# Optimization experiments

Measured on AMD Instinct MI355X. Metric: run time of the kernel, lower is better.

The kernel has to match this reference:

```python
import jax, jax.numpy as jnp
import numpy as np


def _hfft3(x):
    # sequential Hermitian FFT along the 3 spatial axes; each axis n -> 2*(n-1)
    for ax in (2, 3, 4):
        x = jnp.fft.hfft(x, axis=ax)
    return x


def _ihfft3(x):
    # sequential inverse Hermitian FFT; ihfft requires real input, so take real
    # part before each application (mirrors numpy semantics on the original code)
    for ax in (2, 3, 4):
        x = jnp.fft.ihfft(jnp.real(x), axis=ax)
    return x


def setup_inputs() -> dict:
    key = jax.random.key(0)
    k1, k2 = jax.random.split(key)
    B, Cin, Cout = 4, 32, 32
    D1 = D2 = D3 = 64
    m1 = m2 = m3 = 16
    scale = 1.0 / (Cin * Cout)
    x = jax.random.normal(k1, (B, Cin, D1, D2, D3), dtype=jnp.float32)
    weights1 = scale * jax.random.uniform(k2, (Cin, Cout, m1, m2, m3), dtype=jnp.float32)
    return {"x": x, "weights1": weights1}


def reference(x, weights1):
    B = x.shape[0]
    D1, D2, D3 = x.shape[2], x.shape[3], x.shape[4]
    Cout = weights1.shape[1]
    m1, m2, m3 = weights1.shape[2], weights1.shape[3], weights1.shape[4]

    # 3D Hartley-style transform: [B,Cin,2(D1-1),2(D2-1),2(D3-1)] real
    x_ht = _hfft3(x)

    # mode truncation + channel mixing on low modes only
    low = jnp.einsum("bixyz,ioxyz->boxyz", x_ht[:, :, :m1, :m2, :m3], weights1)

    out_ht = jnp.zeros((B, Cout, D1, D2, D3 // 2 + 1), dtype=x.dtype)
    out_ht = out_ht.at[:, :, :m1, :m2, :m3].set(low)

    # inverse transform -> complex [B,Cout,D1//2+1,D2//2+1,(D3//2+1)//2+1]
    out = _ihfft3(out_ht)
    # return real/imag stacked so output is real-valued
    return jnp.stack([out.real, out.imag], axis=-1)
```

## Files before the change

kernel.cpp:

```cpp
#include <hip/hip_runtime.h>
#include <hip/hip_bf16.h>


#define PI2 6.283185307179586476925f

__global__ void k_init(float* __restrict__ Tmat, float* __restrict__ cA,
                       float* __restrict__ cB, float* __restrict__ sB) {
    int t = blockIdx.x * 256 + threadIdx.x;
    if (t < 1024) {
        int k = t >> 6, j = t & 63;
        float w = (j == 0 || j == 63) ? 1.f : 2.f;
        int r = (j * k) % 126;
        Tmat[t] = w * cosf(PI2 * (float)r / 126.f);
    }
    if (t < 528) {
        int p = t >> 4, j = t & 15;
        int r = (j * p) % 64;
        cA[t] = cosf(PI2 * (float)r / 64.f) * (1.f / 64.f);
    }
    if (t < 272) {
        int p = t >> 4, j = t & 15;
        int r = (j * p) % 33;
        float a = PI2 * (float)r / 33.f;
        cB[t] = cosf(a) * (1.f / 33.f);
        sB[t] = sinf(a) * (1.f / 33.f);
    }
}

__global__ __launch_bounds__(256) void k_fwd12(const float* __restrict__ x,
                                               const float* __restrict__ Tmat,
                                               float* __restrict__ A2) {
    __shared__ float xt[64 * 68];
    __shared__ float Ts[16 * 68];
    __shared__ float tmp[16 * 68];
    const int j1 = blockIdx.x, bc = blockIdx.y;
    const int t = threadIdx.x;

    float4* xt4 = (float4*)xt;
    float4* Ts4 = (float4*)Ts;
    const float4* xg = (const float4*)(x + ((size_t)bc * 64 + j1) * 4096);
    for (int c = t; c < 1024; c += 256) {
        int j2 = c >> 4, q = c & 15;
        xt4[j2 * 17 + q] = xg[c];
    }
    if (t < 256) {
        const float4* Tg = (const float4*)Tmat;
        int k = t >> 4, q = t & 15;
        Ts4[k * 17 + q] = Tg[t];
    }
    __syncthreads();

    {
        const int j2 = (t & 15) + 16 * (t >> 6);
        const int k3b = (t >> 4) & 3;
        float acc[4] = {0.f, 0.f, 0.f, 0.f};
#pragma unroll 4
        for (int q = 0; q < 16; q++) {
            float4 xv = xt4[j2 * 17 + q];
#pragma unroll
            for (int c = 0; c < 4; c++) {
                float4 tv = Ts4[(k3b + 4 * c) * 17 + q];
                acc[c] += xv.x * tv.x + xv.y * tv.y + xv.z * tv.z + xv.w * tv.w;
            }
        }
#pragma unroll
        for (int c = 0; c < 4; c++)
            tmp[(k3b + 4 * c) * 68 + j2] = acc[c];
    }
    __syncthreads();

    {
        const int k3 = t & 15;
        const int k2 = t >> 4;
        const float4* tmp4 = (const float4*)tmp;
        float acc = 0.f;
#pragma unroll 4
        for (int q = 0; q < 16; q++) {
            float4 tv = tmp4[k3 * 17 + q];
            float4 Tv = Ts4[k2 * 17 + q];
            acc += tv.x * Tv.x + tv.y * Tv.y + tv.z * Tv.z + tv.w * Tv.w;
        }
        A2[((size_t)bc * 64 + j1) * 256 + t] = acc;
    }
}

__global__ __launch_bounds__(256) void k_fwd3(const float* __restrict__ A2,
                                              const float* __restrict__ Tmat,
                                              float* __restrict__ X) {
    __shared__ float Ts[128];
    const int k1g = blockIdx.x;
    const int bc = blockIdx.y;
    const int t = threadIdx.x;
    if (t < 128) Ts[t] = Tmat[k1g * 128 + t];
    __syncthreads();
    const float* Ap = A2 + (size_t)bc * 64 * 256 + t;
    float a0 = 0.f, a1 = 0.f;
#pragma unroll 8
    for (int j1 = 0; j1 < 64; j1++) {
        float v = Ap[j1 * 256];
        a0 += v * Ts[j1];
        a1 += v * Ts[64 + j1];
    }
    X[(size_t)bc * 4096 + (size_t)(k1g * 2) * 256 + t] = a0;
    X[(size_t)bc * 4096 + (size_t)(k1g * 2 + 1) * 256 + t] = a1;
}

__global__ __launch_bounds__(256) void k_mix(const float* __restrict__ X,
                                             const float* __restrict__ W,
                                             float* __restrict__ low) {
    const int mc = blockIdx.x;
    const int o = blockIdx.y;
    const int m = mc * 256 + threadIdx.x;
    const float* Xp = X + m;
    const float* Wp = W + (size_t)o * 4096 + m;
    float acc[4] = {0.f, 0.f, 0.f, 0.f};
#pragma unroll 4
    for (int i = 0; i < 32; i++) {
        float wv = Wp[(size_t)i * 32 * 4096];
#pragma unroll
        for (int b = 0; b < 4; b++)
            acc[b] += Xp[(size_t)(b * 32 + i) * 4096] * wv;
    }
#pragma unroll
    for (int b = 0; b < 4; b++)
        low[((size_t)(b * 32 + o)) * 4096 + m] = acc[b];
}

__global__ __launch_bounds__(256) void k_inv(const float* __restrict__ low,
                                             const float* __restrict__ cA,
                                             const float* __restrict__ cB,
                                             const float* __restrict__ sB,
                                             float* __restrict__ out) {
    __shared__ float lt[4096];
    __shared__ float c1[256];
    __shared__ float c2[528];
    __shared__ float cAs[528], cBs[272], sBs[272];
    const int p1 = blockIdx.x, bo = blockIdx.y;
    const int t = threadIdx.x;

    float4* lt4 = (float4*)lt;
    const float4* lg = (const float4*)(low + (size_t)bo * 4096);
    for (int c = t; c < 1024; c += 256) lt4[c] = lg[c];
    for (int c = t; c < 528; c += 256) cAs[c] = cA[c];
    for (int c = t; c < 272; c += 256) { cBs[c] = cB[c]; sBs[c] = sB[c]; }
    __syncthreads();

    {
        float acc = 0.f;
#pragma unroll
        for (int k1 = 0; k1 < 16; k1++) acc += lt[(k1 << 8) + t] * cAs[p1 * 16 + k1];
        c1[t] = acc;
    }
    __syncthreads();

    for (int idx = t; idx < 528; idx += 256) {
        int p2 = idx >> 4, k3 = idx & 15;
        float acc = 0.f;
#pragma unroll
        for (int k2 = 0; k2 < 16; k2++) acc += c1[(k2 << 4) + k3] * cAs[p2 * 16 + k2];
        c2[idx] = acc;
    }
    __syncthreads();

    float* op = out + ((size_t)bo * 33 + p1) * 33 * 17 * 2;
    for (int idx = t; idx < 1122; idx += 256) {
        int p2 = idx / 34, rem = idx % 34;
        int p3 = rem >> 1, cc = rem & 1;
        const float* M = cc ? sBs : cBs;
        float acc = 0.f;
#pragma unroll
        for (int k3 = 0; k3 < 16; k3++) acc += c2[(p2 << 4) + k3] * M[p3 * 16 + k3];
        op[idx] = acc;
    }
}

extern "C" void kernel_launch(void* const* d_in, const int* in_sizes, int n_in,
                              void* d_out, int out_size, void* d_ws, size_t ws_size,
                              hipStream_t stream) {
    const float* x = (const float*)d_in[0];
    const float* W = (const float*)d_in[1];
    float* out = (float*)d_out;

    float* ws = (float*)d_ws;
    float* Tmat = ws;
    float* cA   = ws + 1024;
    float* cB   = ws + 1552;
    float* sB   = ws + 1824;
    float* A2   = ws + 4096;
    float* X    = A2 + 2097152;
    float* low  = X + 524288;

    k_init<<<dim3(4), dim3(256), 0, stream>>>(Tmat, cA, cB, sB);
    k_fwd12<<<dim3(64, 128), dim3(256), 0, stream>>>(x, Tmat, A2);
    k_fwd3<<<dim3(8, 128), dim3(256), 0, stream>>>(A2, Tmat, X);
    k_mix<<<dim3(16, 32), dim3(256), 0, stream>>>(X, W, low);
    k_inv<<<dim3(33, 128), dim3(256), 0, stream>>>(low, cA, cB, sB, out);
}
```

Before: 248.2 us.

## Register-tile forward stage, split inverse first stage into its own kernel

The forward 2D stage now runs one 64-thread wavefront per block. Each thread holds its x row in registers and reads the transform matrix directly from global or cache, which removes the large shared-memory transpose staging of x. The inverse transform's first-axis contraction moves into a separate kernel that computes each 256-mode slab once per (b,o). Before, each of the 33 p1 blocks reloaded the full 16KB low tile and recomputed it. This adds an extra launch and a workspace round-trip through U, and the smaller forward blocks may change occupancy and how well the global loads coalesce.

Result: slower. 258.3 us (+4.1%).

```diff
diff --git a/kernel.cpp b/kernel.cpp
--- a/kernel.cpp
+++ b/kernel.cpp
@@ -27,61 +27,58 @@
     }
 }
 
-__global__ __launch_bounds__(256) void k_fwd12(const float* __restrict__ x,
-                                               const float* __restrict__ Tmat,
-                                               float* __restrict__ A2) {
-    __shared__ float xt[64 * 68];
+__global__ __launch_bounds__(64) void k_fwd12(const float* __restrict__ x,
+                                              const float* __restrict__ Tmat,
+                                              float* __restrict__ A2) {
+    __shared__ float tmp[16 * 68];
     __shared__ float Ts[16 * 68];
-    __shared__ float tmp[16 * 68];
     const int j1 = blockIdx.x, bc = blockIdx.y;
     const int t = threadIdx.x;
 
-    float4* xt4 = (float4*)xt;
+    const float4* Tg4 = (const float4*)Tmat;
     float4* Ts4 = (float4*)Ts;
-    const float4* xg = (const float4*)(x + ((size_t)bc * 64 + j1) * 4096);
-    for (int c = t; c < 1024; c += 256) {
-        int j2 = c >> 4, q = c & 15;
-        xt4[j2 * 17 + q] = xg[c];
-    }
-    if (t < 256) {
-        const float4* Tg = (const float4*)Tmat;
-        int k = t >> 4, q = t & 15;
-        Ts4[k * 17 + q] = Tg[t];
-    }
-    __syncthreads();
-
-    {
-        const int j2 = (t & 15) + 16 * (t >> 6);
-        const int k3b = (t >> 4) & 3;
-        float acc[4] = {0.f, 0.f, 0.f, 0.f};
-#pragma unroll 4
+#pragma unroll
+    for (int c = 0; c < 4; c++) {
+        int idx = t + 64 * c;
+        Ts4[(idx >> 4) * 17 + (idx & 15)] = Tg4[idx];
+    }
+
+    const float4* xg = (const float4*)(x + (((size_t)bc * 64 + j1) * 64 + t) * 64);
+    float4 xr[16];
+#pragma unroll
+    for (int q = 0; q < 16; q++) xr[q] = xg[q];
+
+#pragma unroll 2
+    for (int k3 = 0; k3 < 16; k3++) {
+        const float4* Trow = Tg4 + k3 * 16;
+        float ax = 0.f, ay = 0.f, az = 0.f, aw = 0.f;
+#pragma unroll
         for (int q = 0; q < 16; q++) {
-            float4 xv = xt4[j2 * 17 + q];
-#pragma unroll
-            for (int c = 0; c < 4; c++) {
-                float4 tv = Ts4[(k3b + 4 * c) * 17 + q];
-                acc[c] += xv.x * tv.x + xv.y * tv.y + xv.z * tv.z + xv.w * tv.w;
-            }
+            float4 tv = Trow[q];
+            ax += xr[q].x * tv.x;
+            ay += xr[q].y * tv.y;
+            az += xr[q].z * tv.z;
+            aw += xr[q].w * tv.w;
         }
-#pragma unroll
-        for (int c = 0; c < 4; c++)
-            tmp[(k3b + 4 * c) * 68 + j2] = acc[c];
-    }
-    __syncthreads();
-
-    {
-        const int k3 = t & 15;
-        const int k2 = t >> 4;
-        const float4* tmp4 = (const float4*)tmp;
-        float acc = 0.f;
-#pragma unroll 4
-        for (int q = 0; q < 16; q++) {
-            float4 tv = tmp4[k3 * 17 + q];
-            float4 Tv = Ts4[k2 * 17 + q];
-            acc += tv.x * Tv.x + tv.y * Tv.y + tv.z * Tv.z + tv.w * Tv.w;
+        tmp[k3 * 68 + t] = (ax + ay) + (az + aw);
+    }
+    __syncthreads();
+
+    const int k3 = t & 15, k2b = t >> 4;
+    const float4* tmp4 = (const float4*)tmp;
+    float acc2[4] = {0.f, 0.f, 0.f, 0.f};
+#pragma unroll
+    for (int q = 0; q < 16; q++) {
+        float4 tv = tmp4[k3 * 17 + q];
+#pragma unroll
+        for (int c = 0; c < 4; c++) {
+            float4 Tv = Ts4[(k2b + 4 * c) * 17 + q];
+            acc2[c] += tv.x * Tv.x + tv.y * Tv.y + tv.z * Tv.z + tv.w * Tv.w;
         }
-        A2[((size_t)bc * 64 + j1) * 256 + t] = acc;
-    }
+    }
+    float* A2p = A2 + ((size_t)bc * 64 + j1) * 256;
+#pragma unroll
+    for (int c = 0; c < 4; c++) A2p[t + 64 * c] = acc2[c];
 }
 
 __global__ __launch_bounds__(256) void k_fwd3(const float* __restrict__ A2,
@@ -126,31 +123,45 @@
         low[((size_t)(b * 32 + o)) * 4096 + m] = acc[b];
 }
 
-__global__ __launch_bounds__(256) void k_inv(const float* __restrict__ low,
-                                             const float* __restrict__ cA,
-                                             const float* __restrict__ cB,
-                                             const float* __restrict__ sB,
-                                             float* __restrict__ out) {
-    __shared__ float lt[4096];
+__global__ __launch_bounds__(256) void k_invE(const float* __restrict__ low,
+                                              const float* __restrict__ cA,
+                                              float* __restrict__ U) {
+    const int bo = blockIdx.x;
+    const int t = threadIdx.x;
+    const float* lp = low + (size_t)bo * 4096 + t;
+    float lr[16];
+#pragma unroll
+    for (int k1 = 0; k1 < 16; k1++) lr[k1] = lp[k1 << 8];
+    float* up = U + (size_t)bo * 33 * 256 + t;
+#pragma unroll 1
+    for (int p1 = 0; p1 < 33; p1++) {
+        const float* ca = cA + p1 * 16;
+        float a0 = 0.f, a1 = 0.f, a2 = 0.f, a3 = 0.f;
+#pragma unroll
+        for (int k1 = 0; k1 < 16; k1 += 4) {
+            a0 += lr[k1] * ca[k1];
+            a1 += lr[k1 + 1] * ca[k1 + 1];
+            a2 += lr[k1 + 2] * ca[k1 + 2];
+            a3 += lr[k1 + 3] * ca[k1 + 3];
+        }
+        up[p1 * 256] = (a0 + a1) + (a2 + a3);
+    }
+}
+
+__global__ __launch_bounds__(256) void k_invFG(const float* __restrict__ U,
+                                               const float* __restrict__ cA,
+                                               const float* __restrict__ cB,
+                                               const float* __restrict__ sB,
+                                               float* __restrict__ out) {
     __shared__ float c1[256];
     __shared__ float c2[528];
     __shared__ float cAs[528], cBs[272], sBs[272];
     const int p1 = blockIdx.x, bo = blockIdx.y;
     const int t = threadIdx.x;
 
-    float4* lt4 = (float4*)lt;
-    const float4* lg = (const float4*)(low + (size_t)bo * 4096);
-    for (int c = t; c < 1024; c += 256) lt4[c] = lg[c];
+    c1[t] = U[((size_t)bo * 33 + p1) * 256 + t];
     for (int c = t; c < 528; c += 256) cAs[c] = cA[c];
     for (int c = t; c < 272; c += 256) { cBs[c] = cB[c]; sBs[c] = sB[c]; }
-    __syncthreads();
-
-    {
-        float acc = 0.f;
-#pragma unroll
-        for (int k1 = 0; k1 < 16; k1++) acc += lt[(k1 << 8) + t] * cAs[p1 * 16 + k1];
-        c1[t] = acc;
-    }
     __syncthreads();
 
     for (int idx = t; idx < 528; idx += 256) {
@@ -189,10 +200,12 @@
     float* A2   = ws + 4096;
     float* X    = A2 + 2097152;
     float* low  = X + 524288;
+    float* U    = low + 524288;
 
     k_init<<<dim3(4), dim3(256), 0, stream>>>(Tmat, cA, cB, sB);
-    k_fwd12<<<dim3(64, 128), dim3(256), 0, stream>>>(x, Tmat, A2);
+    k_fwd12<<<dim3(64, 128), dim3(64), 0, stream>>>(x, Tmat, A2);
     k_fwd3<<<dim3(8, 128), dim3(256), 0, stream>>>(A2, Tmat, X);
     k_mix<<<dim3(16, 32), dim3(256), 0, stream>>>(X, W, low);
-    k_inv<<<dim3(33, 128), dim3(256), 0, stream>>>(low, cA, cB, sB, out);
-}
+    k_invE<<<dim3(128), dim3(256), 0, stream>>>(low, cA, U);
+    k_invFG<<<dim3(33, 128), dim3(256), 0, stream>>>(U, cA, cB, sB, out);
+}
```

## Coarsen forward and inverse transform kernels with register prefetch and shared stage reuse

Applied to the files above, without the earlier changes.

k_fwd12 now processes 8 j1 slices per block, loading Tmat once and prefetching the next x slice into registers while computing the current one. k_fwd3 computes all 16 k1 outputs per thread in a single block per bc. k_inv runs one block per bo, computing the first-axis transform for all 33 p1 once into shared memory (U1) instead of reloading low per p1. The cost is far fewer blocks (1024 for fwd12, 128 for fwd3 and inv), which reduces occupancy and latency hiding on a GPU with many CUs.

After: 294.7 us. +18.8%, slower.

```diff
diff --git a/kernel.cpp b/kernel.cpp
--- a/kernel.cpp
+++ b/kernel.cpp
@@ -30,79 +30,86 @@
 __global__ __launch_bounds__(256) void k_fwd12(const float* __restrict__ x,
                                                const float* __restrict__ Tmat,
                                                float* __restrict__ A2) {
-    __shared__ float xt[64 * 68];
+    __shared__ float xb[64 * 68];
     __shared__ float Ts[16 * 68];
     __shared__ float tmp[16 * 68];
-    const int j1 = blockIdx.x, bc = blockIdx.y;
+    const int oct = blockIdx.x, bc = blockIdx.y;
     const int t = threadIdx.x;
-
-    float4* xt4 = (float4*)xt;
+    const int j2 = t & 63;
+    const int gu = t >> 6;
+
+    float4* xb4 = (float4*)xb;
     float4* Ts4 = (float4*)Ts;
-    const float4* xg = (const float4*)(x + ((size_t)bc * 64 + j1) * 4096);
-    for (int c = t; c < 1024; c += 256) {
-        int j2 = c >> 4, q = c & 15;
-        xt4[j2 * 17 + q] = xg[c];
-    }
-    if (t < 256) {
-        const float4* Tg = (const float4*)Tmat;
-        int k = t >> 4, q = t & 15;
-        Ts4[k * 17 + q] = Tg[t];
-    }
-    __syncthreads();
-
-    {
-        const int j2 = (t & 15) + 16 * (t >> 6);
-        const int k3b = (t >> 4) & 3;
+    const float4* Tg4 = (const float4*)Tmat;
+
+    Ts4[(t >> 4) * 17 + (t & 15)] = Tg4[t];
+
+    const float4* xg = (const float4*)x + ((size_t)(bc * 64 + oct * 8)) * 1024;
+    float4 pf[4];
+#pragma unroll
+    for (int i = 0; i < 4; i++) pf[i] = xg[t + 256 * i];
+
+    for (int jj = 0; jj < 8; jj++) {
+#pragma unroll
+        for (int i = 0; i < 4; i++) {
+            int idx = t + 256 * i;
+            xb4[(idx >> 4) * 17 + (idx & 15)] = pf[i];
+        }
+        __syncthreads();
+
+        if (jj < 7) {
+            const float4* xn = xg + (size_t)(jj + 1) * 1024;
+#pragma unroll
+            for (int i = 0; i < 4; i++) pf[i] = xn[t + 256 * i];
+        }
+
         float acc[4] = {0.f, 0.f, 0.f, 0.f};
-#pragma unroll 4
+#pragma unroll
         for (int q = 0; q < 16; q++) {
-            float4 xv = xt4[j2 * 17 + q];
+            float4 xv = xb4[j2 * 17 + q];
 #pragma unroll
             for (int c = 0; c < 4; c++) {
-                float4 tv = Ts4[(k3b + 4 * c) * 17 + q];
+                float4 tv = Ts4[(4 * gu + c) * 17 + q];
                 acc[c] += xv.x * tv.x + xv.y * tv.y + xv.z * tv.z + xv.w * tv.w;
             }
         }
 #pragma unroll
-        for (int c = 0; c < 4; c++)
-            tmp[(k3b + 4 * c) * 68 + j2] = acc[c];
-    }
-    __syncthreads();
-
-    {
-        const int k3 = t & 15;
-        const int k2 = t >> 4;
-        const float4* tmp4 = (const float4*)tmp;
-        float acc = 0.f;
-#pragma unroll 4
-        for (int q = 0; q < 16; q++) {
-            float4 tv = tmp4[k3 * 17 + q];
-            float4 Tv = Ts4[k2 * 17 + q];
-            acc += tv.x * Tv.x + tv.y * Tv.y + tv.z * Tv.z + tv.w * Tv.w;
-        }
-        A2[((size_t)bc * 64 + j1) * 256 + t] = acc;
+        for (int c = 0; c < 4; c++) tmp[(4 * gu + c) * 68 + j2] = acc[c];
+        __syncthreads();
+
+        {
+            const int k3 = t & 15, k2 = t >> 4;
+            const float4* tmp4 = (const float4*)tmp;
+            float a2 = 0.f;
+#pragma unroll
+            for (int q = 0; q < 16; q++) {
+                float4 tv = tmp4[k3 * 17 + q];
+                float4 Tv = Ts4[k2 * 17 + q];
+                a2 += tv.x * Tv.x + tv.y * Tv.y + tv.z * Tv.z + tv.w * Tv.w;
+            }
+            A2[((size_t)bc * 64 + oct * 8 + jj) * 256 + t] = a2;
+        }
     }
 }
 
 __global__ __launch_bounds__(256) void k_fwd3(const float* __restrict__ A2,
                                               const float* __restrict__ Tmat,
                                               float* __restrict__ X) {
-    __shared__ float Ts[128];
-    const int k1g = blockIdx.x;
-    const int bc = blockIdx.y;
+    const int bc = blockIdx.x;
     const int t = threadIdx.x;
-    if (t < 128) Ts[t] = Tmat[k1g * 128 + t];
-    __syncthreads();
-    const float* Ap = A2 + (size_t)bc * 64 * 256 + t;
-    float a0 = 0.f, a1 = 0.f;
-#pragma unroll 8
+    const float* Ap = A2 + (size_t)bc * 16384 + t;
+    float acc[16];
+#pragma unroll
+    for (int k = 0; k < 16; k++) acc[k] = 0.f;
+#pragma unroll 4
     for (int j1 = 0; j1 < 64; j1++) {
         float v = Ap[j1 * 256];
-        a0 += v * Ts[j1];
-        a1 += v * Ts[64 + j1];
-    }
-    X[(size_t)bc * 4096 + (size_t)(k1g * 2) * 256 + t] = a0;
-    X[(size_t)bc * 4096 + (size_t)(k1g * 2 + 1) * 256 + t] = a1;
+#pragma unroll
+        for (int k = 0; k < 16; k++) acc[k] += v * Tmat[k * 64 + j1];
+    }
+    float* Xp = X + (size_t)bc * 4096 + t;
+#pragma unroll
+    for (int k = 0; k < 16; k++) Xp[k * 256] = acc[k];
 }
 
 __global__ __launch_bounds__(256) void k_mix(const float* __restrict__ X,
@@ -131,46 +138,58 @@
                                              const float* __restrict__ cB,
                                              const float* __restrict__ sB,
                                              float* __restrict__ out) {
-    __shared__ float lt[4096];
-    __shared__ float c1[256];
+    __shared__ float U1[33 * 256];
     __shared__ float c2[528];
     __shared__ float cAs[528], cBs[272], sBs[272];
-    const int p1 = blockIdx.x, bo = blockIdx.y;
+    const int bo = blockIdx.x;
     const int t = threadIdx.x;
 
-    float4* lt4 = (float4*)lt;
-    const float4* lg = (const float4*)(low + (size_t)bo * 4096);
-    for (int c = t; c < 1024; c += 256) lt4[c] = lg[c];
     for (int c = t; c < 528; c += 256) cAs[c] = cA[c];
     for (int c = t; c < 272; c += 256) { cBs[c] = cB[c]; sBs[c] = sB[c]; }
+
+    const float* lp = low + (size_t)bo * 4096 + t;
+    float lr[16];
+#pragma unroll
+    for (int k1 = 0; k1 < 16; k1++) lr[k1] = lp[k1 << 8];
     __syncthreads();
-
-    {
-        float acc = 0.f;
-#pragma unroll
-        for (int k1 = 0; k1 < 16; k1++) acc += lt[(k1 << 8) + t] * cAs[p1 * 16 + k1];
-        c1[t] = acc;
+#pragma unroll 1
+    for (int p1 = 0; p1 < 33; p1++) {
+        float a0 = 0.f, a1 = 0.f, a2 = 0.f, a3 = 0.f;
+#pragma unroll
+        for (int k1 = 0; k1 < 16; k1 += 4) {
+            a0 += lr[k1] * cAs[p1 * 16 + k1];
+            a1 += lr[k1 + 1] * cAs[p1 * 16 + k1 + 1];
+            a2 += lr[k1 + 2] * cAs[p1 * 16 + k1 + 2];
+            a3 += lr[k1 + 3] * cAs[p1 * 16 + k1 + 3];
+        }
+        U1[p1 * 256 + t] = (a0 + a1) + (a2 + a3);
     }
     __syncthreads();
 
-    for (int idx = t; idx < 528; idx += 256) {
-        int p2 = idx >> 4, k3 = idx & 15;
-        float acc = 0.f;
-#pragma unroll
-        for (int k2 = 0; k2 < 16; k2++) acc += c1[(k2 << 4) + k3] * cAs[p2 * 16 + k2];
-        c2[idx] = acc;
-    }
-    __syncthreads();
-
-    float* op = out + ((size_t)bo * 33 + p1) * 33 * 17 * 2;
-    for (int idx = t; idx < 1122; idx += 256) {
-        int p2 = idx / 34, rem = idx % 34;
-        int p3 = rem >> 1, cc = rem & 1;
-        const float* M = cc ? sBs : cBs;
-        float acc = 0.f;
-#pragma unroll
-        for (int k3 = 0; k3 < 16; k3++) acc += c2[(p2 << 4) + k3] * M[p3 * 16 + k3];
-        op[idx] = acc;
+    float* op = out + (size_t)bo * 33 * 1122;
+#pragma unroll 1
+    for (int p1 = 0; p1 < 33; p1++) {
+        for (int idx = t; idx < 528; idx += 256) {
+            int p2 = idx >> 4, k3 = idx & 15;
+            float acc = 0.f;
+#pragma unroll
+            for (int k2 = 0; k2 < 16; k2++)
+                acc += U1[p1 * 256 + (k2 << 4) + k3] * cAs[p2 * 16 + k2];
+            c2[idx] = acc;
+        }
+        __syncthreads();
+
+        for (int idx = t; idx < 1122; idx += 256) {
+            int p2 = idx / 34, rem = idx % 34;
+            int p3 = rem >> 1, cc = rem & 1;
+            const float* M = cc ? sBs : cBs;
+            float acc = 0.f;
+#pragma unroll
+            for (int k3 = 0; k3 < 16; k3++)
+                acc += c2[(p2 << 4) + k3] * M[p3 * 16 + k3];
+            op[p1 * 1122 + idx] = acc;
+        }
+        __syncthreads();
     }
 }
 
@@ -191,8 +210,8 @@
     float* low  = X + 524288;
 
     k_init<<<dim3(4), dim3(256), 0, stream>>>(Tmat, cA, cB, sB);
-    k_fwd12<<<dim3(64, 128), dim3(256), 0, stream>>>(x, Tmat, A2);
-    k_fwd3<<<dim3(8, 128), dim3(256), 0, stream>>>(A2, Tmat, X);
+    k_fwd12<<<dim3(8, 128), dim3(256), 0, stream>>>(x, Tmat, A2);
+    k_fwd3<<<dim3(128), dim3(256), 0, stream>>>(A2, Tmat, X);
     k_mix<<<dim3(16, 32), dim3(256), 0, stream>>>(X, W, low);
-    k_inv<<<dim3(33, 128), dim3(256), 0, stream>>>(low, cA, cB, sB, out);
-}
+    k_inv<<<dim3(128), dim3(256), 0, stream>>>(low, cA, cB, sB, out);
+}
```
